# Kernel optimization log

Hardware: AMD Instinct MI355X
Metric: run time of the kernel (lower is better)

The kernel has to match this reference:

```python
import jax, jax.numpy as jnp
import numpy as np

B, T, F = 2048, 2048, 16
WINDOW = 24


def _pool_mat(L, S):
    # PyTorch AdaptiveAvgPool1d: bin i averages indices [floor(i*L/S), ceil((i+1)*L/S))
    M = np.zeros((S, L), np.float32)
    for i in range(S):
        s = (i * L) // S
        e = -((-(i + 1) * L) // S)
        M[i, s:e] = 1.0 / (e - s)
    return jnp.asarray(M)


def _conv1d(x, w, dil):
    # x: [B, Cin, L], w: [Cout, Cin, K], VALID, rhs-dilated
    return jax.lax.conv_general_dilated(
        x, w, window_strides=(1,), padding='VALID', rhs_dilation=(dil,),
        dimension_numbers=('NCH', 'OIH', 'NCH'))


def _forward(x, was, wbs, wfc):
    xc = jnp.transpose(x, (0, 2, 1))  # [B, F, T]
    t = x.shape[1]
    feats = []
    for k in range(1, 7):
        # stage a: conv(F->1, kernel k, dil 1) -> adaptive pool to 12 -> leaky relu
        fa = _conv1d(xc, was[k - 1], 1)  # [B, 1, t-k+1]
        fa = jax.nn.leaky_relu(
            jnp.einsum('bcl,sl->bcs', fa, _pool_mat(t - (k - 1), WINDOW // 2)), 0.1)
        # stage b: conv(1->1, kernel k, dil 2) on fa -> adaptive pool to 6 -> leaky relu
        lb = WINDOW // 2 - 2 * (k - 1)  # 12, 10, 8, 6, 4, 2
        fb = _conv1d(fa, wbs[k - 1], 2)  # [B, 1, lb]
        fb = jax.nn.leaky_relu(
            jnp.einsum('bcl,sl->bcs', fb, _pool_mat(lb, WINDOW // 4)), 0.1)
        feats += [fa, fb]  # cat order: f1a, f1b, f2a, f2b, ...
    h = jnp.concatenate(feats, axis=2).reshape(x.shape[0], -1)  # [B, 108]
    return h @ wfc.T  # [B, 1]


def setup_inputs() -> dict:
    key = jax.random.key(0)
    ks = jax.random.split(key, 14)
    inp = {'x': jax.random.normal(ks[0], (B, T, F), jnp.float32)}
    for k in range(1, 7):
        inp[f'wa{k}'] = jax.random.normal(ks[k], (1, F, k), jnp.float32) * 0.1
        inp[f'wb{k}'] = jax.random.normal(ks[6 + k], (1, 1, k), jnp.float32) * 0.3
    inp['wfc'] = jax.random.normal(ks[13], (1, 108), jnp.float32) * 0.1
    return inp


def reference(x, wa1, wa2, wa3, wa4, wa5, wa6,
              wb1, wb2, wb3, wb4, wb5, wb6, wfc):
    was = [wa1, wa2, wa3, wa4, wa5, wa6]
    wbs = [wb1, wb2, wb3, wb4, wb5, wb6]
    return _forward(x, was, wbs, wfc)
```

## Files before the change

kernel.cpp:

```cpp
#include <hip/hip_runtime.h>

#define NCH 16
#define TLEN 2048
#define NTHREADS 256

__global__ __launch_bounds__(NTHREADS, 4) void filternet_kernel(
    const float* __restrict__ x,
    const float* __restrict__ wa1, const float* __restrict__ wa2,
    const float* __restrict__ wa3, const float* __restrict__ wa4,
    const float* __restrict__ wa5, const float* __restrict__ wa6,
    const float* __restrict__ wb1, const float* __restrict__ wb2,
    const float* __restrict__ wb3, const float* __restrict__ wb4,
    const float* __restrict__ wb5, const float* __restrict__ wb6,
    const float* __restrict__ wfc, float* __restrict__ out, int nb)
{
    __shared__ float sA[NTHREADS][NCH + 1];
    __shared__ float sSeg[16][NCH];
    __shared__ float Tt[13 * 16][NCH + 1];
    __shared__ float waL[6][NCH][6];
    __shared__ float wbL[6][6];
    __shared__ float wfcL[108];
    __shared__ float faL[6][12];
    __shared__ float partial[6];

    const int tid = threadIdx.x;
    const int b = blockIdx.x;
    if (b >= nb) return;
    const float* __restrict__ xb = x + (size_t)b * (TLEN * NCH);

    if (tid < 96) {
        const int k0 = tid >> 4, c = tid & 15, K = k0 + 1;
        const float* w = (k0 == 0) ? wa1 : (k0 == 1) ? wa2 : (k0 == 2) ? wa3
                       : (k0 == 3) ? wa4 : (k0 == 4) ? wa5 : wa6;
        for (int j = 0; j < 6; ++j)
            waL[k0][c][j] = (j < K) ? w[c * K + j] : 0.0f;
    } else if (tid < 102) {
        const int k0 = tid - 96, K = k0 + 1;
        const float* w = (k0 == 0) ? wb1 : (k0 == 1) ? wb2 : (k0 == 2) ? wb3
                       : (k0 == 3) ? wb4 : (k0 == 4) ? wb5 : wb6;
        for (int j = 0; j < 6; ++j)
            wbL[k0][j] = (j < K) ? w[j] : 0.0f;
    } else if (tid >= 128 && tid < 236) {
        wfcL[tid - 128] = wfc[tid - 128];
    }

    {
        float accv[NCH];
#pragma unroll
        for (int c = 0; c < NCH; ++c) accv[c] = 0.0f;
        const float4* x4 = reinterpret_cast<const float4*>(xb) + (size_t)tid * 32;
#pragma unroll
        for (int p = 0; p < 8; ++p) {
#pragma unroll
            for (int g = 0; g < 4; ++g) {
                float4 v = x4[p * 4 + g];
                accv[g * 4 + 0] += v.x;
                accv[g * 4 + 1] += v.y;
                accv[g * 4 + 2] += v.z;
                accv[g * 4 + 3] += v.w;
            }
        }
#pragma unroll
        for (int c = 0; c < NCH; ++c) sA[tid][c] = accv[c];
    }
    __syncthreads();

    {
        const int s = tid >> 4, c = tid & 15;
        float v = 0.0f;
#pragma unroll
        for (int u = 0; u < 16; ++u) v += sA[s * 16 + u][c];
        sSeg[s][c] = v;
    }
    __syncthreads();

    if (tid < 13 * 16) {
        const int ci = tid >> 4, c = tid & 15;
        const int cb = (ci == 0) ? 0 : (ci * 2043) / 12 - 1;
        const int j0 = cb >> 3;
        const int sb = j0 >> 4;
        float run = 0.0f;
        for (int s = 0; s < sb; ++s) run += sSeg[s][c];
        for (int j = sb * 16; j < j0; ++j) run += sA[j][c];
        for (int t = j0 * 8; t < cb; ++t) run += xb[(size_t)t * NCH + c];
#pragma unroll
        for (int off = 0; off < 16; ++off) {
            Tt[ci * 16 + off][c] = run;
            const int p = cb + off;
            if (p < TLEN) run += xb[(size_t)p * NCH + c];
        }
    }
    __syncthreads();

    if (tid < 72) {
        const int k0 = tid / 12, i = tid % 12, K = k0 + 1;
        const int L = TLEN - k0;
        const int s = (i * L) / 12;
        const int e = ((i + 1) * L + 11) / 12;
        const int n = e - s;
        const int cbs = (i == 0) ? 0 : (i * 2043) / 12 - 1;
        const int cbe = ((i + 1) * 2043) / 12 - 1;
        const int rs = i * 16 + (s - cbs);
        const int re = (i + 1) * 16 + (e - cbe);
        float acc2 = 0.0f;
        for (int j = 0; j < K; ++j) {
#pragma unroll
            for (int c = 0; c < NCH; ++c)
                acc2 += waL[k0][c][j] * (Tt[re + j][c] - Tt[rs + j][c]);
        }
        float v = acc2 / (float)n;
        faL[k0][i] = (v >= 0.0f) ? v : 0.1f * v;
    }
    __syncthreads();

    if (tid < 6) {
        const int k0 = tid, K = k0 + 1;
        const int lb = 12 - 2 * k0;
        float fbv[12];
        for (int l = 0; l < lb; ++l) {
            float a = 0.0f;
            for (int j = 0; j < K; ++j) a += wbL[k0][j] * faL[k0][l + 2 * j];
            fbv[l] = a;
        }
        float part = 0.0f;
        for (int i2 = 0; i2 < 12; ++i2)
            part += faL[k0][i2] * wfcL[k0 * 18 + i2];
        for (int i6 = 0; i6 < 6; ++i6) {
            const int s6 = (i6 * lb) / 6;
            const int e6 = ((i6 + 1) * lb + 5) / 6;
            float v = 0.0f;
            for (int l = s6; l < e6; ++l) v += fbv[l];
            v /= (float)(e6 - s6);
            v = (v >= 0.0f) ? v : 0.1f * v;
            part += v * wfcL[k0 * 18 + 12 + i6];
        }
        partial[k0] = part;
    }
    __syncthreads();

    if (tid == 0) {
        out[b] = partial[0] + partial[1] + partial[2] +
                 partial[3] + partial[4] + partial[5];
    }
}

extern "C" void kernel_launch(void* const* d_in, const int* in_sizes, int n_in,
                              void* d_out, int out_size, void* d_ws, size_t ws_size,
                              hipStream_t stream) {
    const float* x = nullptr;
    const float* wa[6] = {nullptr};
    const float* wb[6] = {nullptr};
    const float* wfc = nullptr;
    int nb = 0;
    for (int i = 0; i < n_in; ++i) {
        const int sz = in_sizes[i];
        const float* p = (const float*)d_in[i];
        if (sz >= TLEN * NCH) { x = p; nb = sz / (TLEN * NCH); }
        else if (sz == 108)   { wfc = p; }
        else if (sz % NCH == 0 && sz >= NCH && sz <= 6 * NCH) { wa[sz / NCH - 1] = p; }
        else if (sz >= 1 && sz <= 6) { wb[sz - 1] = p; }
    }

    float* outp = (float*)d_out;
    dim3 grid(nb), block(NTHREADS);
    hipLaunchKernelGGL(filternet_kernel, grid, block, 0, stream,
                       x, wa[0], wa[1], wa[2], wa[3], wa[4], wa[5],
                       wb[0], wb[1], wb[2], wb[3], wb[4], wb[5],
                       wfc, outp, nb);
}
```

Measured before the change: 82.43 us.

## Capture prefix windows during streaming load and use wave-shuffle reductions

Each wave now streams a contiguous quarter of the sequence with coalesced float4 loads. It snapshots running sums at the bin boundaries and copies the 16-row windows around each boundary into shared memory as the data passes through. This removes the second global re-read of x in the prefix-table stage and the large shared-memory transpose buffers, and does the reductions with wave shuffles. LDS use drops, so the launch bound is raised to 5 blocks per CU, at the cost of more complex per-iteration predicated stores and extra shuffle work.

```diff
diff --git a/kernel.cpp b/kernel.cpp
--- a/kernel.cpp
+++ b/kernel.cpp
@@ -3,8 +3,9 @@
 #define NCH 16
 #define TLEN 2048
 #define NTHREADS 256
-
-__global__ __launch_bounds__(NTHREADS, 4) void filternet_kernel(
+#define PAD 20
+
+__global__ __launch_bounds__(NTHREADS, 5) void filternet_kernel(
     const float* __restrict__ x,
     const float* __restrict__ wa1, const float* __restrict__ wa2,
     const float* __restrict__ wa3, const float* __restrict__ wa4,
@@ -14,9 +15,9 @@
     const float* __restrict__ wb5, const float* __restrict__ wb6,
     const float* __restrict__ wfc, float* __restrict__ out, int nb)
 {
-    __shared__ float sA[NTHREADS][NCH + 1];
-    __shared__ float sSeg[16][NCH];
-    __shared__ float Tt[13 * 16][NCH + 1];
+    __shared__ float xWin[13 * 16][PAD];
+    __shared__ float sWinBase[13][16];
+    __shared__ float blkSum[4][16];
     __shared__ float waL[6][NCH][6];
     __shared__ float wbL[6][6];
     __shared__ float wfcL[108];
@@ -28,66 +29,103 @@
     if (b >= nb) return;
     const float* __restrict__ xb = x + (size_t)b * (TLEN * NCH);
 
+    const int l  = tid & 63;
+    const int w  = tid >> 6;
+    const int g  = l & 3;
+    const int lq = l >> 2;
+
     if (tid < 96) {
         const int k0 = tid >> 4, c = tid & 15, K = k0 + 1;
-        const float* w = (k0 == 0) ? wa1 : (k0 == 1) ? wa2 : (k0 == 2) ? wa3
-                       : (k0 == 3) ? wa4 : (k0 == 4) ? wa5 : wa6;
+        const float* wv = (k0 == 0) ? wa1 : (k0 == 1) ? wa2 : (k0 == 2) ? wa3
+                        : (k0 == 3) ? wa4 : (k0 == 4) ? wa5 : wa6;
         for (int j = 0; j < 6; ++j)
-            waL[k0][c][j] = (j < K) ? w[c * K + j] : 0.0f;
+            waL[k0][c][j] = (j < K) ? wv[c * K + j] : 0.0f;
     } else if (tid < 102) {
         const int k0 = tid - 96, K = k0 + 1;
-        const float* w = (k0 == 0) ? wb1 : (k0 == 1) ? wb2 : (k0 == 2) ? wb3
-                       : (k0 == 3) ? wb4 : (k0 == 4) ? wb5 : wb6;
+        const float* wv = (k0 == 0) ? wb1 : (k0 == 1) ? wb2 : (k0 == 2) ? wb3
+                        : (k0 == 3) ? wb4 : (k0 == 4) ? wb5 : wb6;
         for (int j = 0; j < 6; ++j)
-            wbL[k0][j] = (j < K) ? w[j] : 0.0f;
+            wbL[k0][j] = (j < K) ? wv[j] : 0.0f;
     } else if (tid >= 128 && tid < 236) {
         wfcL[tid - 128] = wfc[tid - 128];
     }
 
+    int rv[4], qv[4];
+#pragma unroll
+    for (int s = 0; s < 4; ++s) {
+        const int ci = 3 * w + s;
+        const int cb = (ci == 0) ? 0 : (ci * 2043) / 12 - 1;
+        const int r  = cb - (w << 9);
+        rv[s] = r;
+        int q = (r + 15) >> 4;
+        qv[s] = (r >= 0) ? q : -1;
+    }
+
+    float4 acc = make_float4(0.f, 0.f, 0.f, 0.f);
+    float4 sn0 = acc, sn1 = acc, sn2 = acc, sn3 = acc;
+    const float4* x4 = reinterpret_cast<const float4*>(xb) + ((size_t)w * 2048 + l);
+#pragma unroll
+    for (int it = 0; it < 32; ++it) {
+        if (it == qv[0]) sn0 = acc;
+        if (it == qv[1]) sn1 = acc;
+        if (it == qv[2]) sn2 = acc;
+        if (it == qv[3]) sn3 = acc;
+        float4 v = x4[64 * it];
+#pragma unroll
+        for (int s = 0; s < 4; ++s) {
+            const int d = rv[s] - 16 * it;
+            if (d > -16 && d < 16) {
+                const int off = lq - d;
+                if (off >= 0 && off < 16)
+                    *reinterpret_cast<float4*>(&xWin[(3 * w + s) * 16 + off][g * 4]) = v;
+            }
+        }
+        acc.x += v.x; acc.y += v.y; acc.z += v.z; acc.w += v.w;
+    }
+    if (qv[0] == 32) sn0 = acc;
+    if (qv[1] == 32) sn1 = acc;
+    if (qv[2] == 32) sn2 = acc;
+    if (qv[3] == 32) sn3 = acc;
+
     {
-        float accv[NCH];
-#pragma unroll
-        for (int c = 0; c < NCH; ++c) accv[c] = 0.0f;
-        const float4* x4 = reinterpret_cast<const float4*>(xb) + (size_t)tid * 32;
-#pragma unroll
-        for (int p = 0; p < 8; ++p) {
-#pragma unroll
-            for (int g = 0; g < 4; ++g) {
-                float4 v = x4[p * 4 + g];
-                accv[g * 4 + 0] += v.x;
-                accv[g * 4 + 1] += v.y;
-                accv[g * 4 + 2] += v.z;
-                accv[g * 4 + 3] += v.w;
+        float4 t = acc;
+#pragma unroll
+        for (int m = 4; m <= 32; m <<= 1) {
+            t.x += __shfl_xor(t.x, m, 64); t.y += __shfl_xor(t.y, m, 64);
+            t.z += __shfl_xor(t.z, m, 64); t.w += __shfl_xor(t.w, m, 64);
+        }
+        if (l < 4) *reinterpret_cast<float4*>(&blkSum[w][l * 4]) = t;
+    }
+#pragma unroll
+    for (int s = 0; s < 4; ++s) {
+        if (qv[s] >= 0) {
+            float4 t = (s == 0) ? sn0 : (s == 1) ? sn1 : (s == 2) ? sn2 : sn3;
+#pragma unroll
+            for (int m = 4; m <= 32; m <<= 1) {
+                t.x += __shfl_xor(t.x, m, 64); t.y += __shfl_xor(t.y, m, 64);
+                t.z += __shfl_xor(t.z, m, 64); t.w += __shfl_xor(t.w, m, 64);
             }
-        }
-#pragma unroll
-        for (int c = 0; c < NCH; ++c) sA[tid][c] = accv[c];
-    }
-    __syncthreads();
-
-    {
-        const int s = tid >> 4, c = tid & 15;
-        float v = 0.0f;
-#pragma unroll
-        for (int u = 0; u < 16; ++u) v += sA[s * 16 + u][c];
-        sSeg[s][c] = v;
+            if (l < 4) *reinterpret_cast<float4*>(&sWinBase[3 * w + s][l * 4]) = t;
+        }
     }
     __syncthreads();
 
     if (tid < 13 * 16) {
         const int ci = tid >> 4, c = tid & 15;
         const int cb = (ci == 0) ? 0 : (ci * 2043) / 12 - 1;
-        const int j0 = cb >> 3;
-        const int sb = j0 >> 4;
-        float run = 0.0f;
-        for (int s = 0; s < sb; ++s) run += sSeg[s][c];
-        for (int j = sb * 16; j < j0; ++j) run += sA[j][c];
-        for (int t = j0 * 8; t < cb; ++t) run += xb[(size_t)t * NCH + c];
+        const int wb = cb >> 9;
+        const int r  = cb - (wb << 9);
+        const int qc = (r + 15) >> 4;
+        const int ov = (qc << 4) - r;
+        float run = sWinBase[ci][c];
+        for (int wp = 0; wp < wb; ++wp) run += blkSum[wp][c];
+        for (int o = 0; o < ov; ++o) run -= xWin[ci * 16 + o][c];
 #pragma unroll
         for (int off = 0; off < 16; ++off) {
-            Tt[ci * 16 + off][c] = run;
             const int p = cb + off;
-            if (p < TLEN) run += xb[(size_t)p * NCH + c];
+            const float v = xWin[ci * 16 + off][c];
+            xWin[ci * 16 + off][c] = run;
+            if (p < TLEN) run += v;
         }
     }
     __syncthreads();
@@ -106,7 +144,7 @@
         for (int j = 0; j < K; ++j) {
 #pragma unroll
             for (int c = 0; c < NCH; ++c)
-                acc2 += waL[k0][c][j] * (Tt[re + j][c] - Tt[rs + j][c]);
+                acc2 += waL[k0][c][j] * (xWin[re + j][c] - xWin[rs + j][c]);
         }
         float v = acc2 / (float)n;
         faL[k0][i] = (v >= 0.0f) ? v : 0.1f * v;
@@ -117,10 +155,10 @@
         const int k0 = tid, K = k0 + 1;
         const int lb = 12 - 2 * k0;
         float fbv[12];
-        for (int l = 0; l < lb; ++l) {
+        for (int lo = 0; lo < lb; ++lo) {
             float a = 0.0f;
-            for (int j = 0; j < K; ++j) a += wbL[k0][j] * faL[k0][l + 2 * j];
-            fbv[l] = a;
+            for (int j = 0; j < K; ++j) a += wbL[k0][j] * faL[k0][lo + 2 * j];
+            fbv[lo] = a;
         }
         float part = 0.0f;
         for (int i2 = 0; i2 < 12; ++i2)
@@ -129,7 +167,7 @@
             const int s6 = (i6 * lb) / 6;
             const int e6 = ((i6 + 1) * lb + 5) / 6;
             float v = 0.0f;
-            for (int l = s6; l < e6; ++l) v += fbv[l];
+            for (int lo = s6; lo < e6; ++lo) v += fbv[lo];
             v /= (float)(e6 - s6);
             v = (v >= 0.0f) ? v : 0.1f * v;
             part += v * wfcL[k0 * 18 + 12 + i6];
```

After: 314.9 us. 282% more time.
